# Optimization experiments

Hardware: AMD Instinct MI355X
Metric: run time of the kernel (lower is better)

The kernel has to match this reference:

```python
import jax, jax.numpy as jnp
import numpy as np

B, N, C = 8, 131072, 20
K = 20  # max instances per frame (fixed num_segments, replaces int(max()+1) host sync)


def _segment_mean(pts, ids):
    # pts: [N,3], ids: [N] int in [0,K)
    s = jax.ops.segment_sum(pts, ids, num_segments=K)                      # [K,3]
    cnt = jax.ops.segment_sum(jnp.ones((pts.shape[0],), pts.dtype), ids, num_segments=K)  # [K]
    return s / jnp.maximum(cnt, 1.0)[:, None]                              # [K,3]


def setup_inputs() -> dict:
    key = jax.random.key(0)
    k1, k2, k3, k4 = jax.random.split(key, 4)
    points = jax.random.normal(k1, (B, N, 3), dtype=jnp.float32)
    pred_sem_mat = jax.nn.log_softmax(jax.random.normal(k2, (B, N, C), dtype=jnp.float32), axis=-1)
    pred_center_shift_vectors = jax.random.normal(k3, (B, N, 3), dtype=jnp.float32)
    label = jax.random.randint(k4, (B, 2, N), 0, K, dtype=jnp.int64)
    return {"points": points, "pred_sem_mat": pred_sem_mat,
            "pred_center_shift_vectors": pred_center_shift_vectors, "label": label}


def reference(points, pred_sem_mat, pred_center_shift_vectors, label):
    class_gt = label[:, 0, :]      # [B,N]
    instance_gt = label[:, 1, :]   # [B,N]

    # sem loss: F.nll_loss on log-probs = -mean of gathered target log-prob, averaged over frames
    gathered = jnp.take_along_axis(pred_sem_mat, class_gt[..., None], axis=2)[..., 0]  # [B,N]
    sem_loss = -gathered.mean()

    # per-instance centers via segment mean, scattered back per point
    centers = jax.vmap(_segment_mean)(points, instance_gt)                  # [B,K,3]
    center_per_point = jnp.take_along_axis(centers, instance_gt[..., None], axis=1)  # [B,N,3]
    center_shift_vectors_gt = center_per_point - points                     # [B,N,3]

    weight = jnp.minimum(jnp.linalg.norm(center_shift_vectors_gt, axis=2), 1.0)  # [B,N]
    csv_loss = (jnp.linalg.norm(center_shift_vectors_gt - pred_center_shift_vectors, axis=2) * weight).mean()

    return sem_loss + 0.2 * csv_loss
```

## Files before the change

kernel.cpp:

```cpp
#include <hip/hip_runtime.h>
#include <hip/hip_bf16.h>

#define Bn 8
#define Nn 131072
#define Cn 20
#define Kn 20

#define THREADS 256
#define GRID 2048
#define BLOCKS_PER_BATCH (GRID / Bn)
#define CHUNK (Nn / BLOCKS_PER_BATCH)
#define EPB (CHUNK / THREADS)

#define NREP 8
#define RSTRIDE 84

#define WS_SEG 0
#define WS_SEMP 640
#define WS_CSVP (640 + GRID)
#define WS_ZERO_FLOATS 640

__global__ void __launch_bounds__(THREADS) loss_pass1(
    const float* __restrict__ points,
    const float* __restrict__ sem,
    const int* __restrict__ label,
    float* __restrict__ ws) {
    __shared__ float acc[NREP][RSTRIDE];
    __shared__ float wsum[4];

    const int tid  = threadIdx.x;
    const int wave = tid >> 6;
    const int lane = tid & 63;
    const int rep  = lane & (NREP - 1);

    for (int i = tid; i < NREP * RSTRIDE; i += THREADS) ((float*)acc)[i] = 0.0f;
    __syncthreads();

    const int b  = blockIdx.x / BLOCKS_PER_BATCH;
    const int n0 = (blockIdx.x % BLOCKS_PER_BATCH) * CHUNK;
    const int* lab = label + (long)b * 2 * Nn;

    float semsum = 0.0f;
#pragma unroll
    for (int e = 0; e < EPB; ++e) {
        const int n    = n0 + e * THREADS + tid;
        const int cls  = lab[n];
        const int inst = lab[Nn + n];
        const long rowb = (long)b * Nn + n;
        semsum += __builtin_nontemporal_load(&sem[rowb * Cn + cls]);
        const float3 p = ((const float3*)points)[rowb];
        float* a = acc[rep];
        atomicAdd(&a[0 * 21 + inst], p.x);
        atomicAdd(&a[1 * 21 + inst], p.y);
        atomicAdd(&a[2 * 21 + inst], p.z);
        atomicAdd(&a[3 * 21 + inst], 1.0f);
    }
    __syncthreads();

    if (tid < Kn * 4) {
        const int k = tid >> 2, f = tid & 3;
        float v = 0.0f;
#pragma unroll
        for (int r = 0; r < NREP; ++r) v += acc[r][f * 21 + k];
        atomicAdd(&ws[WS_SEG + (b * Kn + k) * 4 + f], v);
    }

#pragma unroll
    for (int off = 32; off > 0; off >>= 1) semsum += __shfl_down(semsum, off);
    if (lane == 0) wsum[wave] = semsum;
    __syncthreads();
    if (tid == 0) ws[WS_SEMP + blockIdx.x] = wsum[0] + wsum[1] + wsum[2] + wsum[3];
}

__global__ void __launch_bounds__(THREADS) loss_pass2(
    const float* __restrict__ points,
    const float* __restrict__ pcsv,
    const int* __restrict__ label,
    float* __restrict__ ws) {
    __shared__ float ctr[Kn][3];
    __shared__ float wsum[4];

    const int tid  = threadIdx.x;
    const int wave = tid >> 6;
    const int lane = tid & 63;
    const int b    = blockIdx.x / BLOCKS_PER_BATCH;

    if (tid < Kn) {
        const float* s = ws + WS_SEG + (b * Kn + tid) * 4;
        const float inv = 1.0f / fmaxf(s[3], 1.0f);
        ctr[tid][0] = s[0] * inv;
        ctr[tid][1] = s[1] * inv;
        ctr[tid][2] = s[2] * inv;
    }
    __syncthreads();

    const int n0 = (blockIdx.x % BLOCKS_PER_BATCH) * CHUNK;
    const int* inst_lab = label + (long)b * 2 * Nn + Nn;

    float lsum = 0.0f;
#pragma unroll
    for (int e = 0; e < EPB; ++e) {
        const int n    = n0 + e * THREADS + tid;
        const int inst = inst_lab[n];
        const long rowb = (long)b * Nn + n;
        const float3 p = ((const float3*)points)[rowb];
        const float3 q = ((const float3*)pcsv)[rowb];
        const float dx = ctr[inst][0] - p.x;
        const float dy = ctr[inst][1] - p.y;
        const float dz = ctr[inst][2] - p.z;
        const float nd = sqrtf(dx * dx + dy * dy + dz * dz);
        const float w  = fminf(nd, 1.0f);
        const float ex = dx - q.x;
        const float ey = dy - q.y;
        const float ez = dz - q.z;
        lsum += sqrtf(ex * ex + ey * ey + ez * ez) * w;
    }

#pragma unroll
    for (int off = 32; off > 0; off >>= 1) lsum += __shfl_down(lsum, off);
    if (lane == 0) wsum[wave] = lsum;
    __syncthreads();
    if (tid == 0) ws[WS_CSVP + blockIdx.x] = wsum[0] + wsum[1] + wsum[2] + wsum[3];
}

__global__ void __launch_bounds__(THREADS) loss_final(
    const float* __restrict__ ws, float* __restrict__ out) {
    __shared__ float ssum[4], csum[4];
    const int tid  = threadIdx.x;
    const int wave = tid >> 6;
    const int lane = tid & 63;

    float s = 0.0f, c = 0.0f;
#pragma unroll
    for (int i = 0; i < GRID / THREADS; ++i) {
        s += ws[WS_SEMP + i * THREADS + tid];
        c += ws[WS_CSVP + i * THREADS + tid];
    }
#pragma unroll
    for (int off = 32; off > 0; off >>= 1) {
        s += __shfl_down(s, off);
        c += __shfl_down(c, off);
    }
    if (lane == 0) { ssum[wave] = s; csum[wave] = c; }
    __syncthreads();
    if (tid == 0) {
        const float S = ssum[0] + ssum[1] + ssum[2] + ssum[3];
        const float C = csum[0] + csum[1] + csum[2] + csum[3];
        const float invBN = 1.0f / (float)((long)Bn * Nn);
        out[0] = -S * invBN + 0.2f * C * invBN;
    }
}

extern "C" void kernel_launch(void* const* d_in, const int* in_sizes, int n_in,
                              void* d_out, int out_size, void* d_ws, size_t ws_size,
                              hipStream_t stream) {
    const float* points = (const float*)d_in[0];
    const float* sem    = (const float*)d_in[1];
    const float* pcsv   = (const float*)d_in[2];
    const int*   label  = (const int*)d_in[3];
    float* ws  = (float*)d_ws;
    float* out = (float*)d_out;

    hipMemsetAsync(d_ws, 0, WS_ZERO_FLOATS * sizeof(float), stream);
    loss_pass1<<<GRID, THREADS, 0, stream>>>(points, sem, label, ws);
    loss_pass2<<<GRID, THREADS, 0, stream>>>(points, pcsv, label, ws);
    loss_final<<<1, THREADS, 0, stream>>>(ws, out);
}
```

Measured before the change: 158.1 us.

## Fuse three loss kernels into one cooperative kernel with grid syncs

Replaces the memset plus three separate kernel launches with a single cooperative kernel that uses grid.sync between the segment-sum, center-loss and final reduction phases. Points and instance labels are kept in registers from the first phase, so the second phase does not reload them. The grid is halved to 1024 blocks so all blocks can be co-resident, which doubles the work per thread. This removes launch overhead and redundant global reads, at the cost of three grid-wide barriers and higher register pressure.

```diff
diff --git a/kernel.cpp b/kernel.cpp
--- a/kernel.cpp
+++ b/kernel.cpp
@@ -1,5 +1,7 @@
 #include <hip/hip_runtime.h>
-#include <hip/hip_bf16.h>
+#include <hip/hip_cooperative_groups.h>
+
+namespace cg = cooperative_groups;
 
 #define Bn 8
 #define Nn 131072
@@ -7,7 +9,7 @@
 #define Kn 20
 
 #define THREADS 256
-#define GRID 2048
+#define GRID 1024
 #define BLOCKS_PER_BATCH (GRID / Bn)
 #define CHUNK (Nn / BLOCKS_PER_BATCH)
 #define EPB (CHUNK / THREADS)
@@ -17,43 +19,53 @@
 
 #define WS_SEG 0
 #define WS_SEMP 640
-#define WS_CSVP (640 + GRID)
-#define WS_ZERO_FLOATS 640
+#define WS_CSVP (WS_SEMP + GRID)
 
-__global__ void __launch_bounds__(THREADS) loss_pass1(
+__global__ void __launch_bounds__(THREADS, 4) loss_fused(
     const float* __restrict__ points,
     const float* __restrict__ sem,
+    const float* __restrict__ pcsv,
     const int* __restrict__ label,
-    float* __restrict__ ws) {
+    float* __restrict__ ws,
+    float* __restrict__ out) {
+    cg::grid_group grid = cg::this_grid();
+
     __shared__ float acc[NREP][RSTRIDE];
     __shared__ float wsum[4];
+    __shared__ float ctr[Kn][3];
 
     const int tid  = threadIdx.x;
     const int wave = tid >> 6;
     const int lane = tid & 63;
     const int rep  = lane & (NREP - 1);
+    const int bid  = blockIdx.x;
+    const int b    = bid / BLOCKS_PER_BATCH;
+    const int n0   = (bid % BLOCKS_PER_BATCH) * CHUNK;
 
     for (int i = tid; i < NREP * RSTRIDE; i += THREADS) ((float*)acc)[i] = 0.0f;
+    if (bid == 0) {
+        for (int i = tid; i < Bn * Kn * 4; i += THREADS) ws[WS_SEG + i] = 0.0f;
+    }
     __syncthreads();
+    grid.sync();
 
-    const int b  = blockIdx.x / BLOCKS_PER_BATCH;
-    const int n0 = (blockIdx.x % BLOCKS_PER_BATCH) * CHUNK;
     const int* lab = label + (long)b * 2 * Nn;
-
     float semsum = 0.0f;
+    float3 p[EPB];
+    int inst[EPB];
 #pragma unroll
     for (int e = 0; e < EPB; ++e) {
         const int n    = n0 + e * THREADS + tid;
         const int cls  = lab[n];
-        const int inst = lab[Nn + n];
+        inst[e] = lab[Nn + n];
         const long rowb = (long)b * Nn + n;
         semsum += __builtin_nontemporal_load(&sem[rowb * Cn + cls]);
-        const float3 p = ((const float3*)points)[rowb];
+        p[e] = ((const float3*)points)[rowb];
         float* a = acc[rep];
-        atomicAdd(&a[0 * 21 + inst], p.x);
-        atomicAdd(&a[1 * 21 + inst], p.y);
-        atomicAdd(&a[2 * 21 + inst], p.z);
-        atomicAdd(&a[3 * 21 + inst], 1.0f);
+        atomicAdd(&a[0 * 21 + inst[e]], p[e].x);
+        atomicAdd(&a[1 * 21 + inst[e]], p[e].y);
+        atomicAdd(&a[2 * 21 + inst[e]], p[e].z);
+        atomicAdd(&a[3 * 21 + inst[e]], 1.0f);
     }
     __syncthreads();
 
@@ -65,25 +77,14 @@
         atomicAdd(&ws[WS_SEG + (b * Kn + k) * 4 + f], v);
     }
 
+    float s1 = semsum;
 #pragma unroll
-    for (int off = 32; off > 0; off >>= 1) semsum += __shfl_down(semsum, off);
-    if (lane == 0) wsum[wave] = semsum;
+    for (int off = 32; off > 0; off >>= 1) s1 += __shfl_down(s1, off);
+    if (lane == 0) wsum[wave] = s1;
     __syncthreads();
-    if (tid == 0) ws[WS_SEMP + blockIdx.x] = wsum[0] + wsum[1] + wsum[2] + wsum[3];
-}
+    if (tid == 0) ws[WS_SEMP + bid] = wsum[0] + wsum[1] + wsum[2] + wsum[3];
 
-__global__ void __launch_bounds__(THREADS) loss_pass2(
-    const float* __restrict__ points,
-    const float* __restrict__ pcsv,
-    const int* __restrict__ label,
-    float* __restrict__ ws) {
-    __shared__ float ctr[Kn][3];
-    __shared__ float wsum[4];
-
-    const int tid  = threadIdx.x;
-    const int wave = tid >> 6;
-    const int lane = tid & 63;
-    const int b    = blockIdx.x / BLOCKS_PER_BATCH;
+    grid.sync();
 
     if (tid < Kn) {
         const float* s = ws + WS_SEG + (b * Kn + tid) * 4;
@@ -94,20 +95,16 @@
     }
     __syncthreads();
 
-    const int n0 = (blockIdx.x % BLOCKS_PER_BATCH) * CHUNK;
-    const int* inst_lab = label + (long)b * 2 * Nn + Nn;
-
     float lsum = 0.0f;
 #pragma unroll
     for (int e = 0; e < EPB; ++e) {
         const int n    = n0 + e * THREADS + tid;
-        const int inst = inst_lab[n];
         const long rowb = (long)b * Nn + n;
-        const float3 p = ((const float3*)points)[rowb];
         const float3 q = ((const float3*)pcsv)[rowb];
-        const float dx = ctr[inst][0] - p.x;
-        const float dy = ctr[inst][1] - p.y;
-        const float dz = ctr[inst][2] - p.z;
+        const int k = inst[e];
+        const float dx = ctr[k][0] - p[e].x;
+        const float dy = ctr[k][1] - p[e].y;
+        const float dz = ctr[k][2] - p[e].z;
         const float nd = sqrtf(dx * dx + dy * dy + dz * dz);
         const float w  = fminf(nd, 1.0f);
         const float ex = dx - q.x;
@@ -115,39 +112,35 @@
         const float ez = dz - q.z;
         lsum += sqrtf(ex * ex + ey * ey + ez * ez) * w;
     }
-
 #pragma unroll
     for (int off = 32; off > 0; off >>= 1) lsum += __shfl_down(lsum, off);
     if (lane == 0) wsum[wave] = lsum;
     __syncthreads();
-    if (tid == 0) ws[WS_CSVP + blockIdx.x] = wsum[0] + wsum[1] + wsum[2] + wsum[3];
-}
+    if (tid == 0) ws[WS_CSVP + bid] = wsum[0] + wsum[1] + wsum[2] + wsum[3];
 
-__global__ void __launch_bounds__(THREADS) loss_final(
-    const float* __restrict__ ws, float* __restrict__ out) {
-    __shared__ float ssum[4], csum[4];
-    const int tid  = threadIdx.x;
-    const int wave = tid >> 6;
-    const int lane = tid & 63;
+    grid.sync();
 
-    float s = 0.0f, c = 0.0f;
+    if (bid == 0) {
+        float s = 0.0f, c = 0.0f;
 #pragma unroll
-    for (int i = 0; i < GRID / THREADS; ++i) {
-        s += ws[WS_SEMP + i * THREADS + tid];
-        c += ws[WS_CSVP + i * THREADS + tid];
-    }
+        for (int i = 0; i < GRID / THREADS; ++i) {
+            s += ws[WS_SEMP + i * THREADS + tid];
+            c += ws[WS_CSVP + i * THREADS + tid];
+        }
 #pragma unroll
-    for (int off = 32; off > 0; off >>= 1) {
-        s += __shfl_down(s, off);
-        c += __shfl_down(c, off);
-    }
-    if (lane == 0) { ssum[wave] = s; csum[wave] = c; }
-    __syncthreads();
-    if (tid == 0) {
-        const float S = ssum[0] + ssum[1] + ssum[2] + ssum[3];
-        const float C = csum[0] + csum[1] + csum[2] + csum[3];
-        const float invBN = 1.0f / (float)((long)Bn * Nn);
-        out[0] = -S * invBN + 0.2f * C * invBN;
+        for (int off = 32; off > 0; off >>= 1) {
+            s += __shfl_down(s, off);
+            c += __shfl_down(c, off);
+        }
+        __shared__ float ssum[4], csum[4];
+        if (lane == 0) { ssum[wave] = s; csum[wave] = c; }
+        __syncthreads();
+        if (tid == 0) {
+            const float S = ssum[0] + ssum[1] + ssum[2] + ssum[3];
+            const float C = csum[0] + csum[1] + csum[2] + csum[3];
+            const float invBN = 1.0f / (float)((long)Bn * Nn);
+            out[0] = -S * invBN + 0.2f * C * invBN;
+        }
     }
 }
 
@@ -161,8 +154,9 @@
     float* ws  = (float*)d_ws;
     float* out = (float*)d_out;
 
-    hipMemsetAsync(d_ws, 0, WS_ZERO_FLOATS * sizeof(float), stream);
-    loss_pass1<<<GRID, THREADS, 0, stream>>>(points, sem, label, ws);
-    loss_pass2<<<GRID, THREADS, 0, stream>>>(points, pcsv, label, ws);
-    loss_final<<<1, THREADS, 0, stream>>>(ws, out);
+    void* args[] = { (void*)&points, (void*)&sem, (void*)&pcsv,
+                     (void*)&label, (void*)&ws, (void*)&out };
+    hipLaunchCooperativeKernel((const void*)loss_fused,
+                               dim3(GRID), dim3(THREADS),
+                               args, 0, stream);
 }
```

After: 419.8 us. 2.65x slower.

## Replace global atomics and memset with per-block partial bins reduced in pass2

Applied to the files above, without the earlier changes.

Pass1 no longer does global atomicAdds into 640 shared segment slots. Each block instead writes its 80 per-instance partial sums to a dedicated slot, and pass2 reduces those partials per batch before computing centers. This removes the hipMemsetAsync launch and the contention on global atomics. Both passes also drop from 2048 to 1024 blocks, which doubles the work per thread. In exchange, every pass2 block redundantly sums 128 partials for each of its 80 bins.

```diff
diff --git a/kernel.cpp b/kernel.cpp
--- a/kernel.cpp
+++ b/kernel.cpp
@@ -7,18 +7,23 @@
 #define Kn 20
 
 #define THREADS 256
-#define GRID 2048
-#define BLOCKS_PER_BATCH (GRID / Bn)
-#define CHUNK (Nn / BLOCKS_PER_BATCH)
-#define EPB (CHUNK / THREADS)
+
+#define GRID1 1024
+#define BPB1 (GRID1 / Bn)
+#define CHUNK1 (Nn / BPB1)
+#define EPB1 (CHUNK1 / THREADS)
+
+#define GRID2 1024
+#define BPB2 (GRID2 / Bn)
+#define CHUNK2 (Nn / BPB2)
+#define EPB2 (CHUNK2 / THREADS)
 
 #define NREP 8
 #define RSTRIDE 84
 
-#define WS_SEG 0
-#define WS_SEMP 640
-#define WS_CSVP (640 + GRID)
-#define WS_ZERO_FLOATS 640
+#define WS_BIN 0
+#define WS_SEMP (80 * GRID1)
+#define WS_CSVP (WS_SEMP + GRID1)
 
 __global__ void __launch_bounds__(THREADS) loss_pass1(
     const float* __restrict__ points,
@@ -32,17 +37,18 @@
     const int wave = tid >> 6;
     const int lane = tid & 63;
     const int rep  = lane & (NREP - 1);
+    const int bid  = blockIdx.x;
 
     for (int i = tid; i < NREP * RSTRIDE; i += THREADS) ((float*)acc)[i] = 0.0f;
     __syncthreads();
 
-    const int b  = blockIdx.x / BLOCKS_PER_BATCH;
-    const int n0 = (blockIdx.x % BLOCKS_PER_BATCH) * CHUNK;
+    const int b  = bid / BPB1;
+    const int n0 = (bid % BPB1) * CHUNK1;
     const int* lab = label + (long)b * 2 * Nn;
 
     float semsum = 0.0f;
 #pragma unroll
-    for (int e = 0; e < EPB; ++e) {
+    for (int e = 0; e < EPB1; ++e) {
         const int n    = n0 + e * THREADS + tid;
         const int cls  = lab[n];
         const int inst = lab[Nn + n];
@@ -57,19 +63,19 @@
     }
     __syncthreads();
 
-    if (tid < Kn * 4) {
-        const int k = tid >> 2, f = tid & 3;
+    if (tid < 80) {
+        const int f = tid / 20, k = tid % 20;
         float v = 0.0f;
 #pragma unroll
         for (int r = 0; r < NREP; ++r) v += acc[r][f * 21 + k];
-        atomicAdd(&ws[WS_SEG + (b * Kn + k) * 4 + f], v);
+        ws[WS_BIN + tid * GRID1 + bid] = v;
     }
 
 #pragma unroll
     for (int off = 32; off > 0; off >>= 1) semsum += __shfl_down(semsum, off);
     if (lane == 0) wsum[wave] = semsum;
     __syncthreads();
-    if (tid == 0) ws[WS_SEMP + blockIdx.x] = wsum[0] + wsum[1] + wsum[2] + wsum[3];
+    if (tid == 0) ws[WS_SEMP + bid] = wsum[0] + wsum[1] + wsum[2] + wsum[3];
 }
 
 __global__ void __launch_bounds__(THREADS) loss_pass2(
@@ -77,29 +83,38 @@
     const float* __restrict__ pcsv,
     const int* __restrict__ label,
     float* __restrict__ ws) {
+    __shared__ float sums[80];
     __shared__ float ctr[Kn][3];
     __shared__ float wsum[4];
 
     const int tid  = threadIdx.x;
     const int wave = tid >> 6;
     const int lane = tid & 63;
-    const int b    = blockIdx.x / BLOCKS_PER_BATCH;
+    const int bid  = blockIdx.x;
+    const int b    = bid / BPB2;
 
+    if (tid < 80) {
+        const float* src = ws + WS_BIN + tid * GRID1 + b * BPB1;
+        float v = 0.0f;
+#pragma unroll 8
+        for (int j = 0; j < BPB1; ++j) v += src[j];
+        sums[tid] = v;
+    }
+    __syncthreads();
     if (tid < Kn) {
-        const float* s = ws + WS_SEG + (b * Kn + tid) * 4;
-        const float inv = 1.0f / fmaxf(s[3], 1.0f);
-        ctr[tid][0] = s[0] * inv;
-        ctr[tid][1] = s[1] * inv;
-        ctr[tid][2] = s[2] * inv;
+        const float inv = 1.0f / fmaxf(sums[3 * 20 + tid], 1.0f);
+        ctr[tid][0] = sums[0 * 20 + tid] * inv;
+        ctr[tid][1] = sums[1 * 20 + tid] * inv;
+        ctr[tid][2] = sums[2 * 20 + tid] * inv;
     }
     __syncthreads();
 
-    const int n0 = (blockIdx.x % BLOCKS_PER_BATCH) * CHUNK;
+    const int n0 = (bid % BPB2) * CHUNK2;
     const int* inst_lab = label + (long)b * 2 * Nn + Nn;
 
     float lsum = 0.0f;
 #pragma unroll
-    for (int e = 0; e < EPB; ++e) {
+    for (int e = 0; e < EPB2; ++e) {
         const int n    = n0 + e * THREADS + tid;
         const int inst = inst_lab[n];
         const long rowb = (long)b * Nn + n;
@@ -120,7 +135,7 @@
     for (int off = 32; off > 0; off >>= 1) lsum += __shfl_down(lsum, off);
     if (lane == 0) wsum[wave] = lsum;
     __syncthreads();
-    if (tid == 0) ws[WS_CSVP + blockIdx.x] = wsum[0] + wsum[1] + wsum[2] + wsum[3];
+    if (tid == 0) ws[WS_CSVP + bid] = wsum[0] + wsum[1] + wsum[2] + wsum[3];
 }
 
 __global__ void __launch_bounds__(THREADS) loss_final(
@@ -132,10 +147,9 @@
 
     float s = 0.0f, c = 0.0f;
 #pragma unroll
-    for (int i = 0; i < GRID / THREADS; ++i) {
-        s += ws[WS_SEMP + i * THREADS + tid];
-        c += ws[WS_CSVP + i * THREADS + tid];
-    }
+    for (int i = 0; i < GRID1 / THREADS; ++i) s += ws[WS_SEMP + i * THREADS + tid];
+#pragma unroll
+    for (int i = 0; i < GRID2 / THREADS; ++i) c += ws[WS_CSVP + i * THREADS + tid];
 #pragma unroll
     for (int off = 32; off > 0; off >>= 1) {
         s += __shfl_down(s, off);
@@ -161,8 +175,7 @@
     float* ws  = (float*)d_ws;
     float* out = (float*)d_out;
 
-    hipMemsetAsync(d_ws, 0, WS_ZERO_FLOATS * sizeof(float), stream);
-    loss_pass1<<<GRID, THREADS, 0, stream>>>(points, sem, label, ws);
-    loss_pass2<<<GRID, THREADS, 0, stream>>>(points, pcsv, label, ws);
+    loss_pass1<<<GRID1, THREADS, 0, stream>>>(points, sem, label, ws);
+    loss_pass2<<<GRID2, THREADS, 0, stream>>>(points, pcsv, label, ws);
     loss_final<<<1, THREADS, 0, stream>>>(ws, out);
 }
```

Result: no change. 157.0 us (-0.7%).
